# Kernel tuning notes

Hardware: AMD Instinct MI355X
Metric: run time of the kernel (lower is better)

Reference implementation:

```python
import jax, jax.numpy as jnp
import numpy as np

MODEL_DIM = 256
PAIR_IMPORTANCE_WEIGHT = 0.5
B, S, D = 4, 4096, MODEL_DIM


def setup_inputs() -> dict:
    key = jax.random.key(0)
    ks = jax.random.split(key, 6)
    return {
        "query": jax.random.normal(ks[0], (B, S, D), dtype=jnp.float32),
        "key": jax.random.normal(ks[1], (B, S, D), dtype=jnp.float32),
        "value": jax.random.normal(ks[2], (B, S, D), dtype=jnp.float32),
        "W_query": jax.random.normal(ks[3], (D, D), dtype=jnp.float32),
        "W_key": jax.random.normal(ks[4], (D, D), dtype=jnp.float32),
        "W_value": jax.random.normal(ks[5], (D, D), dtype=jnp.float32),
    }


def reference(query, key, value, W_query, W_key, W_value):
    # Projections: [B,S,D] @ [D,D]
    q = jnp.einsum('bsd,de->bse', query, W_query)
    k = jnp.einsum('bsd,de->bse', key, W_key)
    v = jnp.einsum('bsd,de->bse', value, W_value)
    scale = jnp.sqrt(jnp.asarray(MODEL_DIM, dtype=q.dtype))
    # Full [B,S,S] score matrix (global max forces materialization)
    scores = jnp.einsum('bqd,bkd->bqk', q, k) / scale
    s_len = scores.shape[1]
    diag_bias = jnp.eye(s_len, dtype=scores.dtype) * jnp.max(scores)
    scores = scores + PAIR_IMPORTANCE_WEIGHT * diag_bias  # broadcast over batch
    attention_weights = jax.nn.softmax(scores, axis=-1)
    output = jnp.einsum('bqk,bkd->bqd', attention_weights, v)
    return output, attention_weights
```

## Files before the change

### kernel.cpp

```cpp
#include <hip/hip_runtime.h>
#include <cstdint>
#include <cstddef>

#define BB 4
#define SS 4096
#define DD 256
#define SCORE_SCALE (1.0f/16.0f)
#define PIW 0.5f
#define NROWS (BB * SS)

typedef float          f32x4  __attribute__((ext_vector_type(4)));
typedef __bf16         bf16v8 __attribute__((ext_vector_type(8)));
typedef unsigned short u16v8  __attribute__((ext_vector_type(8)));
typedef unsigned short u16v4  __attribute__((ext_vector_type(4)));

__device__ __forceinline__ f32x4 mfma_bf16(u16v8 a, u16v8 b, f32x4 c) {
    return __builtin_amdgcn_mfma_f32_16x16x32_bf16(
        __builtin_bit_cast(bf16v8, a), __builtin_bit_cast(bf16v8, b), c, 0, 0, 0);
}

__device__ __forceinline__ unsigned short f2bf(float f) {
    unsigned u = __float_as_uint(f);
    u += 0x7FFFu + ((u >> 16) & 1u);
    return (unsigned short)(u >> 16);
}
__device__ __forceinline__ float bf2f(unsigned short h) {
    return __uint_as_float(((unsigned)h) << 16);
}
__device__ __forceinline__ unsigned fenc(float x) {
    unsigned u = __float_as_uint(x);
    return (u & 0x80000000u) ? ~u : (u | 0x80000000u);
}
__device__ __forceinline__ float fdec(unsigned e) {
    return __uint_as_float((e & 0x80000000u) ? (e ^ 0x80000000u) : ~e);
}

__device__ __forceinline__ size_t fragidx(int growFlat, int k, int kPerRow32) {
    return ((((size_t)(growFlat >> 4) * kPerRow32 + (k >> 5)) * 64)
            + ((growFlat & 15) | (((k >> 3) & 3) << 4))) * 8 + (k & 7);
}

#define PSPAD 42

__global__ __launch_bounds__(256) void proj_kernel(
    const float* __restrict__ query, const float* __restrict__ key_, const float* __restrict__ value,
    const float* __restrict__ Wq, const float* __restrict__ Wk, const float* __restrict__ Wv,
    unsigned short* __restrict__ qh, unsigned short* __restrict__ ql,
    unsigned short* __restrict__ kh, unsigned short* __restrict__ kl,
    unsigned short* __restrict__ vT, unsigned* __restrict__ gmax)
{
    const int z = blockIdx.z;
    const float* A = (z == 0) ? query : (z == 1) ? key_ : value;
    const float* W = (z == 0) ? Wq    : (z == 1) ? Wk   : Wv;
    if (z == 0 && blockIdx.x == 0 && blockIdx.y == 0 && threadIdx.x == 0)
        *gmax = 0x007FFFFFu;

    __shared__ unsigned short Ah[128][PSPAD];
    __shared__ unsigned short Al[128][PSPAD];
    __shared__ unsigned short Bh[128][PSPAD];
    __shared__ unsigned short Bl[128][PSPAD];

    const int tid = threadIdx.x;
    const int lane = tid & 63, w = tid >> 6;
    const int wr = (w >> 1) * 64, wc = (w & 1) * 64;
    const int m = lane & 15, qq = lane >> 4;
    const int rowBase = blockIdx.y * 128;
    const int colBase = blockIdx.x * 128;

    f32x4 acc[4][4];
    #pragma unroll
    for (int i = 0; i < 4; i++)
        #pragma unroll
        for (int j = 0; j < 4; j++)
            acc[i][j] = (f32x4){0.f, 0.f, 0.f, 0.f};

    const int chunk = (tid & 3) * 8;
    const int srow  = tid >> 2;

    for (int k0 = 0; k0 < DD; k0 += 32) {
        #pragma unroll
        for (int i = 0; i < 2; i++) {
            int r = srow + i * 64;
            const float* src = &A[(size_t)(rowBase + r) * DD + k0 + chunk];
            float4 f0 = *(const float4*)src;
            float4 f1 = *(const float4*)(src + 4);
            float v[8] = {f0.x, f0.y, f0.z, f0.w, f1.x, f1.y, f1.z, f1.w};
            u16v8 h, l;
            #pragma unroll
            for (int e = 0; e < 8; e++) {
                h[e] = f2bf(v[e]);
                l[e] = f2bf(v[e] - bf2f(h[e]));
            }
            *(u16v8*)&Ah[r][chunk] = h;
            *(u16v8*)&Al[r][chunk] = l;
        }
        #pragma unroll
        for (int i = 0; i < 4; i++) {
            int idx = tid + i * 256;
            int kk = idx >> 5, nq = idx & 31;
            float4 f = *(const float4*)&W[(size_t)(k0 + kk) * DD + colBase + nq * 4];
            float v[4] = {f.x, f.y, f.z, f.w};
            #pragma unroll
            for (int e = 0; e < 4; e++) {
                unsigned short h = f2bf(v[e]);
                unsigned short l = f2bf(v[e] - bf2f(h));
                Bh[nq * 4 + e][kk] = h;
                Bl[nq * 4 + e][kk] = l;
            }
        }
        __syncthreads();

        const int kb = qq * 8;
        u16v8 ah[4], al[4], bh[4], bl[4];
        #pragma unroll
        for (int i = 0; i < 4; i++) {
            ah[i] = *(const u16v8*)&Ah[wr + i * 16 + m][kb];
            al[i] = *(const u16v8*)&Al[wr + i * 16 + m][kb];
            bh[i] = *(const u16v8*)&Bh[wc + i * 16 + m][kb];
            bl[i] = *(const u16v8*)&Bl[wc + i * 16 + m][kb];
        }
        #pragma unroll
        for (int i = 0; i < 4; i++)
            #pragma unroll
            for (int j = 0; j < 4; j++) {
                acc[i][j] = mfma_bf16(ah[i], bh[j], acc[i][j]);
                acc[i][j] = mfma_bf16(ah[i], bl[j], acc[i][j]);
                acc[i][j] = mfma_bf16(al[i], bh[j], acc[i][j]);
            }
        __syncthreads();
    }

    #pragma unroll
    for (int i = 0; i < 4; i++) {
        #pragma unroll
        for (int j = 0; j < 4; j++) {
            #pragma unroll
            for (int r = 0; r < 4; r++) {
                const int gr  = rowBase + wr + i * 16 + qq * 4 + r;
                const int col = colBase + wc + j * 16 + m;
                const float v = acc[i][j][r];
                if (z == 2) {
                    const int b2 = gr >> 12, s2 = gr & (SS - 1);
                    size_t idx = (size_t)b2 * (16 * 128 * 512)
                               + fragidx(col, s2, 128);
                    vT[idx] = f2bf(v);
                } else {
                    unsigned short h = f2bf(v);
                    unsigned short l = f2bf(v - bf2f(h));
                    unsigned short* H = (z == 0) ? qh : kh;
                    unsigned short* L = (z == 0) ? ql : kl;
                    size_t idx = fragidx(gr, col, 8);
                    H[idx] = h;
                    L[idx] = l;
                }
            }
        }
    }
}

__global__ __launch_bounds__(256) void scores_mfma(
    const unsigned short* __restrict__ qh, const unsigned short* __restrict__ ql,
    const unsigned short* __restrict__ kh, const unsigned short* __restrict__ kl,
    float* __restrict__ attn, unsigned* __restrict__ gmax,
    float* __restrict__ tmaxg, float* __restrict__ tsumg)
{
    const int lin = blockIdx.x;
    const int b = (lin & 7) >> 1;
    const int t2 = ((lin >> 3) << 1) | (lin & 1);
    const int bx = t2 & 31, by = t2 >> 5;
    const int rowBase = by * 128;
    const int colBase = bx * 128;

    float* C = attn + (size_t)b * SS * SS;

    __shared__ float s_m[4][64];
    __shared__ float s_s[4][64];
    __shared__ float red[128];

    const int tid = threadIdx.x;
    const int lane = tid & 63, w = tid >> 6;
    const int wr = (w >> 1) * 64, wc = (w & 1) * 64;
    const int m = lane & 15, qq = lane >> 4;

    f32x4 acc[4][4];
    #pragma unroll
    for (int i = 0; i < 4; i++)
        #pragma unroll
        for (int j = 0; j < 4; j++)
            acc[i][j] = (f32x4){0.f, 0.f, 0.f, 0.f};

    const size_t ta = ((size_t)b * SS + rowBase + wr) >> 4;
    const size_t tb = ((size_t)b * SS + colBase + wc) >> 4;

    #pragma unroll 2
    for (int kk = 0; kk < 8; kk++) {
        u16v8 ah[4], al[4], bh[4], bl[4];
        #pragma unroll
        for (int i = 0; i < 4; i++) {
            const size_t fa = (((ta + i) * 8 + kk) * 64 + lane) * 8;
            const size_t fb = (((tb + i) * 8 + kk) * 64 + lane) * 8;
            ah[i] = *(const u16v8*)&qh[fa];
            al[i] = *(const u16v8*)&ql[fa];
            bh[i] = *(const u16v8*)&kh[fb];
            bl[i] = *(const u16v8*)&kl[fb];
        }
        #pragma unroll
        for (int i = 0; i < 4; i++)
            #pragma unroll
            for (int j = 0; j < 4; j++) {
                acc[i][j] = mfma_bf16(ah[i], bh[j], acc[i][j]);
                acc[i][j] = mfma_bf16(ah[i], bl[j], acc[i][j]);
                acc[i][j] = mfma_bf16(al[i], bh[j], acc[i][j]);
            }
    }

    #pragma unroll
    for (int i = 0; i < 4; i++)
        #pragma unroll
        for (int j = 0; j < 4; j++)
            acc[i][j] *= SCORE_SCALE;

    float lmax[16];
    #pragma unroll
    for (int i = 0; i < 4; i++)
        #pragma unroll
        for (int r = 0; r < 4; r++)
            lmax[i * 4 + r] = fmaxf(fmaxf(acc[i][0][r], acc[i][1][r]),
                                    fmaxf(acc[i][2][r], acc[i][3][r]));
    #pragma unroll
    for (int t = 0; t < 16; t++) {
        #pragma unroll
        for (int msk = 1; msk < 16; msk <<= 1)
            lmax[t] = fmaxf(lmax[t], __shfl_xor(lmax[t], msk));
    }
    if (m == 0) {
        #pragma unroll
        for (int i = 0; i < 4; i++)
            #pragma unroll
            for (int r = 0; r < 4; r++)
                s_m[w][i * 16 + qq * 4 + r] = lmax[i * 4 + r];
    }
    __syncthreads();
    float lsum[16];
    #pragma unroll
    for (int i = 0; i < 4; i++)
        #pragma unroll
        for (int r = 0; r < 4; r++) {
            int idx = i * 16 + qq * 4 + r;
            float rm = fmaxf(s_m[w][idx], s_m[w ^ 1][idx]);
            float s = 0.f;
            #pragma unroll
            for (int j = 0; j < 4; j++)
                s += __expf(acc[i][j][r] - rm);
            lsum[i * 4 + r] = s;
        }
    #pragma unroll
    for (int t = 0; t < 16; t++) {
        #pragma unroll
        for (int msk = 1; msk < 16; msk <<= 1)
            lsum[t] += __shfl_xor(lsum[t], msk);
    }
    if (m == 0) {
        #pragma unroll
        for (int i = 0; i < 4; i++)
            #pragma unroll
            for (int r = 0; r < 4; r++)
                s_s[w][i * 16 + qq * 4 + r] = lsum[i * 4 + r];
    }
    __syncthreads();

    if (tid < 128) {
        int wp = tid >> 6, lr = tid & 63;
        float tm = fmaxf(s_m[2 * wp][lr], s_m[2 * wp + 1][lr]);
        float ts = s_s[2 * wp][lr] + s_s[2 * wp + 1][lr];
        size_t gi = (size_t)bx * NROWS + (size_t)b * SS + rowBase + tid;
        tmaxg[gi] = tm;
        tsumg[gi] = ts;
        red[tid] = tm;
    }
    __syncthreads();
    for (int s2 = 64; s2 > 0; s2 >>= 1) {
        if (tid < s2) red[tid] = fmaxf(red[tid], red[tid + s2]);
        __syncthreads();
    }
    if (tid == 0) atomicMax(gmax, fenc(red[0]));

    #pragma unroll
    for (int i = 0; i < 4; i++)
        #pragma unroll
        for (int j = 0; j < 4; j++)
            #pragma unroll
            for (int r = 0; r < 4; r++) {
                int row = rowBase + wr + i * 16 + qq * 4 + r;
                int col = colBase + wc + j * 16 + m;
                __builtin_nontemporal_store(acc[i][j][r], &C[(size_t)row * SS + col]);
            }
}

__global__ __launch_bounds__(256) void stats_merge(
    const float* __restrict__ tmaxg, const float* __restrict__ tsumg,
    const float* __restrict__ attn, const unsigned* __restrict__ gmax,
    float* __restrict__ rowm, float* __restrict__ rowinv)
{
    const int grow = blockIdx.x * 256 + threadIdx.x;
    const int b = grow >> 12, i = grow & (SS - 1);
    const float bias = PIW * fdec(*gmax);

    float tm[32];
    float mx = -INFINITY;
    #pragma unroll
    for (int t = 0; t < 32; t++) {
        tm[t] = tmaxg[(size_t)t * NROWS + grow];
        mx = fmaxf(mx, tm[t]);
    }
    const float dii = attn[(size_t)b * SS * SS + (size_t)i * SS + i];
    mx = fmaxf(mx, dii + bias);

    float s = 0.f;
    #pragma unroll
    for (int t = 0; t < 32; t++)
        s += tsumg[(size_t)t * NROWS + grow] * __expf(tm[t] - mx);
    s += __expf(dii + bias - mx) - __expf(dii - mx);

    rowm[grow] = mx;
    rowinv[grow] = 1.0f / s;
}

#define AVBK 256

__global__ __launch_bounds__(256) void av_softmax_mfma(
    float* __restrict__ attn, const unsigned short* __restrict__ vT,
    const float* __restrict__ rowm, const float* __restrict__ rowinv,
    const unsigned* __restrict__ gmax, float* __restrict__ out)
{
    const int lin = blockIdx.x;
    const int b = (lin & 7) >> 1;
    const int rowTile = ((lin >> 3) << 1) | (lin & 1);
    const int rowBase = rowTile * 32;

    float* A = attn + (size_t)b * SS * SS;
    const unsigned short* Bf = vT + (size_t)b * (16 * 128 * 512);
    const float bias = PIW * fdec(*gmax);

    __shared__ unsigned short As[2][32][264];

    const int tid = threadIdx.x;
    const int lane = tid & 63, w = tid >> 6;
    const int m = lane & 15, qq = lane >> 4;

    const int ra = tid >> 3;
    const int c8 = tid & 7;
    const int rr = rowBase + ra;
    float* Arow = A + (size_t)rr * SS;
    const float mr = rowm[b * SS + rr];
    const float ri = rowinv[b * SS + rr];

    f32x4 acc[2][4];
    #pragma unroll
    for (int i = 0; i < 2; i++)
        #pragma unroll
        for (int j = 0; j < 4; j++)
            acc[i][j] = (f32x4){0.f, 0.f, 0.f, 0.f};

    f32x4 pf[8];

    auto loadA = [&](int kbase) {
        #pragma unroll
        for (int u = 0; u < 8; u++)
            pf[u] = *(const f32x4*)&Arow[kbase + c8 * 4 + u * 32];
    };
    auto procStore = [&](int kbase, int buf) {
        #pragma unroll
        for (int u = 0; u < 8; u++) {
            int c = c8 * 4 + u * 32;
            int j0 = kbase + c;
            float e0 = pf[u][0] + ((j0 + 0 == rr) ? bias : 0.0f);
            float e1 = pf[u][1] + ((j0 + 1 == rr) ? bias : 0.0f);
            float e2 = pf[u][2] + ((j0 + 2 == rr) ? bias : 0.0f);
            float e3 = pf[u][3] + ((j0 + 3 == rr) ? bias : 0.0f);
            float w0 = __expf(e0 - mr) * ri;
            float w1 = __expf(e1 - mr) * ri;
            float w2 = __expf(e2 - mr) * ri;
            float w3 = __expf(e3 - mr) * ri;
            f32x4 wv = (f32x4){w0, w1, w2, w3};
            __builtin_nontemporal_store(wv, (f32x4*)&Arow[j0]);
            *(u16v4*)&As[buf][ra][c] =
                (u16v4){f2bf(w0), f2bf(w1), f2bf(w2), f2bf(w3)};
        }
    };

    const int NT = SS / AVBK;

    loadA(0);
    procStore(0, 0);
    __syncthreads();

    for (int t = 0; t < NT; t++) {
        const int k0 = t * AVBK;
        const int cur = t & 1;
        if (t + 1 < NT)
            loadA(k0 + AVBK);
        #pragma unroll
        for (int kk = 0; kk < 8; kk++) {
            const int kb = kk * 32 + qq * 8;
            const int kkg = (k0 >> 5) + kk;
            u16v8 bf_[4], af_[2];
            #pragma unroll
            for (int j = 0; j < 4; j++)
                bf_[j] = *(const u16v8*)&Bf[(((size_t)(w * 4 + j) * 128 + kkg) * 64 + lane) * 8];
            #pragma unroll
            for (int i = 0; i < 2; i++)
                af_[i] = *(const u16v8*)&As[cur][i * 16 + m][kb];
            #pragma unroll
            for (int i = 0; i < 2; i++)
                #pragma unroll
                for (int j = 0; j < 4; j++)
                    acc[i][j] = mfma_bf16(af_[i], bf_[j], acc[i][j]);
        }
        if (t + 1 < NT) {
            procStore(k0 + AVBK, cur ^ 1);
            __syncthreads();
        }
    }

    #pragma unroll
    for (int i = 0; i < 2; i++) {
        #pragma unroll
        for (int j = 0; j < 4; j++) {
            #pragma unroll
            for (int r = 0; r < 4; r++) {
                int row = rowBase + i * 16 + qq * 4 + r;
                int col = w * 64 + j * 16 + m;
                __builtin_nontemporal_store(
                    acc[i][j][r], &out[((size_t)b * SS + row) * DD + col]);
            }
        }
    }
}

extern "C" void kernel_launch(void* const* d_in, const int* in_sizes, int n_in,
                              void* d_out, int out_size, void* d_ws, size_t ws_size,
                              hipStream_t stream)
{
    const float* query = (const float*)d_in[0];
    const float* key_  = (const float*)d_in[1];
    const float* value = (const float*)d_in[2];
    const float* Wq    = (const float*)d_in[3];
    const float* Wk    = (const float*)d_in[4];
    const float* Wv    = (const float*)d_in[5];

    float* out  = (float*)d_out;
    float* attn = out + (size_t)BB * SS * DD;

    const size_t E = (size_t)BB * SS * DD;
    unsigned short* qh = (unsigned short*)d_ws;
    unsigned short* ql = qh + E;
    unsigned short* kh = ql + E;
    unsigned short* kl = kh + E;
    unsigned short* vT = kl + E;
    float* tmaxg  = (float*)(vT + E);
    float* tsumg  = tmaxg + 32 * (size_t)NROWS;
    float* rowm   = tsumg + 32 * (size_t)NROWS;
    float* rowinv = rowm + NROWS;
    unsigned* gmax = (unsigned*)(rowinv + NROWS);

    proj_kernel<<<dim3(DD / 128, (BB * SS) / 128, 3), 256, 0, stream>>>(
        query, key_, value, Wq, Wk, Wv, qh, ql, kh, kl, vT, gmax);
    scores_mfma<<<dim3(4096), 256, 0, stream>>>(
        qh, ql, kh, kl, attn, gmax, tmaxg, tsumg);
    stats_merge<<<dim3(NROWS / 256), 256, 0, stream>>>(
        tmaxg, tsumg, attn, gmax, rowm, rowinv);
    av_softmax_mfma<<<dim3(512), 256, 0, stream>>>(
        attn, vT, rowm, rowinv, gmax, out);
}
```

Baseline: 615.4 us.

## Stage projection epilogue through LDS, double-buffer score loads, widen AV LDS stores

The projection epilogue now writes its results into shared memory and then emits 16-byte vectorized global stores in the fragment layout, replacing scattered 2-byte stores (V goes through a transposed staging path). The scores kernel double-buffers its fragment loads from global memory across k-steps so that loads for the next step overlap the MFMAs of the current one. The AV softmax kernel loads and stores 8 contiguous elements per thread with 16-byte LDS writes and a wider row pad. The costs are extra LDS traffic and barriers, plus higher register pressure from the doubled fragment buffers.

```diff
diff --git a/kernel.cpp b/kernel.cpp
--- a/kernel.cpp
+++ b/kernel.cpp
@@ -41,6 +41,7 @@
 }
 
 #define PSPAD 42
+#define TRW 136
 
 __global__ __launch_bounds__(256) void proj_kernel(
     const float* __restrict__ query, const float* __restrict__ key_, const float* __restrict__ value,
@@ -55,10 +56,11 @@
     if (z == 0 && blockIdx.x == 0 && blockIdx.y == 0 && threadIdx.x == 0)
         *gmax = 0x007FFFFFu;
 
-    __shared__ unsigned short Ah[128][PSPAD];
-    __shared__ unsigned short Al[128][PSPAD];
-    __shared__ unsigned short Bh[128][PSPAD];
-    __shared__ unsigned short Bl[128][PSPAD];
+    __shared__ __align__(16) unsigned short smem[4 * 128 * PSPAD];
+    unsigned short* Ah = smem;
+    unsigned short* Al = smem + 128 * PSPAD;
+    unsigned short* Bh = smem + 2 * 128 * PSPAD;
+    unsigned short* Bl = smem + 3 * 128 * PSPAD;
 
     const int tid = threadIdx.x;
     const int lane = tid & 63, w = tid >> 6;
@@ -91,8 +93,8 @@
                 h[e] = f2bf(v[e]);
                 l[e] = f2bf(v[e] - bf2f(h[e]));
             }
-            *(u16v8*)&Ah[r][chunk] = h;
-            *(u16v8*)&Al[r][chunk] = l;
+            *(u16v8*)&Ah[r * PSPAD + chunk] = h;
+            *(u16v8*)&Al[r * PSPAD + chunk] = l;
         }
         #pragma unroll
         for (int i = 0; i < 4; i++) {
@@ -104,8 +106,8 @@
             for (int e = 0; e < 4; e++) {
                 unsigned short h = f2bf(v[e]);
                 unsigned short l = f2bf(v[e] - bf2f(h));
-                Bh[nq * 4 + e][kk] = h;
-                Bl[nq * 4 + e][kk] = l;
+                Bh[(nq * 4 + e) * PSPAD + kk] = h;
+                Bl[(nq * 4 + e) * PSPAD + kk] = l;
             }
         }
         __syncthreads();
@@ -114,10 +116,10 @@
         u16v8 ah[4], al[4], bh[4], bl[4];
         #pragma unroll
         for (int i = 0; i < 4; i++) {
-            ah[i] = *(const u16v8*)&Ah[wr + i * 16 + m][kb];
-            al[i] = *(const u16v8*)&Al[wr + i * 16 + m][kb];
-            bh[i] = *(const u16v8*)&Bh[wc + i * 16 + m][kb];
-            bl[i] = *(const u16v8*)&Bl[wc + i * 16 + m][kb];
+            ah[i] = *(const u16v8*)&Ah[(wr + i * 16 + m) * PSPAD + kb];
+            al[i] = *(const u16v8*)&Al[(wr + i * 16 + m) * PSPAD + kb];
+            bh[i] = *(const u16v8*)&Bh[(wc + i * 16 + m) * PSPAD + kb];
+            bl[i] = *(const u16v8*)&Bl[(wc + i * 16 + m) * PSPAD + kb];
         }
         #pragma unroll
         for (int i = 0; i < 4; i++)
@@ -130,30 +132,67 @@
         __syncthreads();
     }
 
-    #pragma unroll
-    for (int i = 0; i < 4; i++) {
-        #pragma unroll
-        for (int j = 0; j < 4; j++) {
-            #pragma unroll
-            for (int r = 0; r < 4; r++) {
-                const int gr  = rowBase + wr + i * 16 + qq * 4 + r;
-                const int col = colBase + wc + j * 16 + m;
-                const float v = acc[i][j][r];
-                if (z == 2) {
-                    const int b2 = gr >> 12, s2 = gr & (SS - 1);
-                    size_t idx = (size_t)b2 * (16 * 128 * 512)
-                               + fragidx(col, s2, 128);
-                    vT[idx] = f2bf(v);
-                } else {
+    if (z == 2) {
+        #pragma unroll
+        for (int i = 0; i < 4; i++)
+            #pragma unroll
+            for (int j = 0; j < 4; j++)
+                #pragma unroll
+                for (int r = 0; r < 4; r++)
+                    smem[(wc + j * 16 + m) * TRW + (wr + i * 16 + qq * 4 + r)] =
+                        f2bf(acc[i][j][r]);
+        __syncthreads();
+        #pragma unroll
+        for (int p = 0; p < 8; p++) {
+            int u_ = tid + p * 256;
+            int dl = u_ >> 4, sg = u_ & 15;
+            u16v8 v = *(const u16v8*)&smem[dl * TRW + sg * 8];
+            int col = colBase + dl;
+            int grS = rowBase + sg * 8;
+            int b2 = grS >> 12, s2 = grS & (SS - 1);
+            size_t idx = (size_t)b2 * (16 * 128 * 512) + fragidx(col, s2, 128);
+            *(u16v8*)&vT[idx] = v;
+        }
+    } else {
+        unsigned short* H = (z == 0) ? qh : kh;
+        unsigned short* L = (z == 0) ? ql : kl;
+        #pragma unroll
+        for (int i = 0; i < 4; i++)
+            #pragma unroll
+            for (int j = 0; j < 4; j++)
+                #pragma unroll
+                for (int r = 0; r < 4; r++)
+                    smem[(wr + i * 16 + qq * 4 + r) * TRW + (wc + j * 16 + m)] =
+                        f2bf(acc[i][j][r]);
+        __syncthreads();
+        #pragma unroll
+        for (int p = 0; p < 8; p++) {
+            int u_ = tid + p * 256;
+            int row = u_ >> 4, kg = u_ & 15;
+            u16v8 v = *(const u16v8*)&smem[row * TRW + kg * 8];
+            size_t idx = fragidx(rowBase + row, colBase + kg * 8, 8);
+            *(u16v8*)&H[idx] = v;
+        }
+        __syncthreads();
+        #pragma unroll
+        for (int i = 0; i < 4; i++)
+            #pragma unroll
+            for (int j = 0; j < 4; j++)
+                #pragma unroll
+                for (int r = 0; r < 4; r++) {
+                    float v = acc[i][j][r];
                     unsigned short h = f2bf(v);
-                    unsigned short l = f2bf(v - bf2f(h));
-                    unsigned short* H = (z == 0) ? qh : kh;
-                    unsigned short* L = (z == 0) ? ql : kl;
-                    size_t idx = fragidx(gr, col, 8);
-                    H[idx] = h;
-                    L[idx] = l;
+                    smem[(wr + i * 16 + qq * 4 + r) * TRW + (wc + j * 16 + m)] =
+                        f2bf(v - bf2f(h));
                 }
-            }
+        __syncthreads();
+        #pragma unroll
+        for (int p = 0; p < 8; p++) {
+            int u_ = tid + p * 256;
+            int row = u_ >> 4, kg = u_ & 15;
+            u16v8 v = *(const u16v8*)&smem[row * TRW + kg * 8];
+            size_t idx = fragidx(rowBase + row, colBase + kg * 8, 8);
+            *(u16v8*)&L[idx] = v;
         }
     }
 }
@@ -192,27 +231,34 @@
     const size_t ta = ((size_t)b * SS + rowBase + wr) >> 4;
     const size_t tb = ((size_t)b * SS + colBase + wc) >> 4;
 
-    #pragma unroll 2
+    u16v8 ah[2][4], al[2][4], bh[2][4], bl[2][4];
+
+    #define SC_LOAD(s, kkv)                                                   \
+        _Pragma("unroll")                                                     \
+        for (int i = 0; i < 4; i++) {                                         \
+            const size_t fa = (((ta + i) * 8 + (kkv)) * 64 + lane) * 8;       \
+            const size_t fb = (((tb + i) * 8 + (kkv)) * 64 + lane) * 8;       \
+            ah[s][i] = *(const u16v8*)&qh[fa];                                \
+            al[s][i] = *(const u16v8*)&ql[fa];                                \
+            bh[s][i] = *(const u16v8*)&kh[fb];                                \
+            bl[s][i] = *(const u16v8*)&kl[fb];                                \
+        }
+
+    SC_LOAD(0, 0)
+    #pragma unroll
     for (int kk = 0; kk < 8; kk++) {
-        u16v8 ah[4], al[4], bh[4], bl[4];
-        #pragma unroll
-        for (int i = 0; i < 4; i++) {
-            const size_t fa = (((ta + i) * 8 + kk) * 64 + lane) * 8;
-            const size_t fb = (((tb + i) * 8 + kk) * 64 + lane) * 8;
-            ah[i] = *(const u16v8*)&qh[fa];
-            al[i] = *(const u16v8*)&ql[fa];
-            bh[i] = *(const u16v8*)&kh[fb];
-            bl[i] = *(const u16v8*)&kl[fb];
-        }
+        const int cur = kk & 1;
+        if (kk < 7) { SC_LOAD(cur ^ 1, kk + 1) }
         #pragma unroll
         for (int i = 0; i < 4; i++)
             #pragma unroll
             for (int j = 0; j < 4; j++) {
-                acc[i][j] = mfma_bf16(ah[i], bh[j], acc[i][j]);
-                acc[i][j] = mfma_bf16(ah[i], bl[j], acc[i][j]);
-                acc[i][j] = mfma_bf16(al[i], bh[j], acc[i][j]);
-            }
-    }
+                acc[i][j] = mfma_bf16(ah[cur][i], bh[cur][j], acc[i][j]);
+                acc[i][j] = mfma_bf16(ah[cur][i], bl[cur][j], acc[i][j]);
+                acc[i][j] = mfma_bf16(al[cur][i], bh[cur][j], acc[i][j]);
+            }
+    }
+    #undef SC_LOAD
 
     #pragma unroll
     for (int i = 0; i < 4; i++)
@@ -327,6 +373,7 @@
 }
 
 #define AVBK 256
+#define ASW 272
 
 __global__ __launch_bounds__(256) void av_softmax_mfma(
     float* __restrict__ attn, const unsigned short* __restrict__ vT,
@@ -342,7 +389,7 @@
     const unsigned short* Bf = vT + (size_t)b * (16 * 128 * 512);
     const float bias = PIW * fdec(*gmax);
 
-    __shared__ unsigned short As[2][32][264];
+    __shared__ __align__(16) unsigned short As[2][32][ASW];
 
     const int tid = threadIdx.x;
     const int lane = tid & 63, w = tid >> 6;
@@ -366,26 +413,30 @@
 
     auto loadA = [&](int kbase) {
         #pragma unroll
-        for (int u = 0; u < 8; u++)
-            pf[u] = *(const f32x4*)&Arow[kbase + c8 * 4 + u * 32];
+        for (int g = 0; g < 4; g++) {
+            pf[2 * g]     = *(const f32x4*)&Arow[kbase + g * 64 + c8 * 8];
+            pf[2 * g + 1] = *(const f32x4*)&Arow[kbase + g * 64 + c8 * 8 + 4];
+        }
     };
     auto procStore = [&](int kbase, int buf) {
         #pragma unroll
-        for (int u = 0; u < 8; u++) {
-            int c = c8 * 4 + u * 32;
+        for (int g = 0; g < 4; g++) {
+            int c = g * 64 + c8 * 8;
             int j0 = kbase + c;
-            float e0 = pf[u][0] + ((j0 + 0 == rr) ? bias : 0.0f);
-            float e1 = pf[u][1] + ((j0 + 1 == rr) ? bias : 0.0f);
-            float e2 = pf[u][2] + ((j0 + 2 == rr) ? bias : 0.0f);
-            float e3 = pf[u][3] + ((j0 + 3 == rr) ? bias : 0.0f);
-            float w0 = __expf(e0 - mr) * ri;
-            float w1 = __expf(e1 - mr) * ri;
-            float w2 = __expf(e2 - mr) * ri;
-            float w3 = __expf(e3 - mr) * ri;
-            f32x4 wv = (f32x4){w0, w1, w2, w3};
-            __builtin_nontemporal_store(wv, (f32x4*)&Arow[j0]);
-            *(u16v4*)&As[buf][ra][c] =
-                (u16v4){f2bf(w0), f2bf(w1), f2bf(w2), f2bf(w3)};
+            float wv[8];
+            #pragma unroll
+            for (int e = 0; e < 8; e++) {
+                float x = (e < 4) ? pf[2 * g][e] : pf[2 * g + 1][e & 3];
+                x += ((j0 + e) == rr) ? bias : 0.0f;
+                wv[e] = __expf(x - mr) * ri;
+            }
+            __builtin_nontemporal_store((f32x4){wv[0], wv[1], wv[2], wv[3]},
+                                        (f32x4*)&Arow[j0]);
+            __builtin_nontemporal_store((f32x4){wv[4], wv[5], wv[6], wv[7]},
+                                        (f32x4*)&Arow[j0 + 4]);
+            *(u16v8*)&As[buf][ra][c] =
+                (u16v8){f2bf(wv[0]), f2bf(wv[1]), f2bf(wv[2]), f2bf(wv[3]),
+                        f2bf(wv[4]), f2bf(wv[5]), f2bf(wv[6]), f2bf(wv[7])};
         }
     };
 
```

Measured after the change: 792.5 us. 28.8% more time.
